# Performance work log

Measured on AMD Instinct MI355X. Metric: run time of the kernel, lower is better.

## Reference

```python
import jax, jax.numpy as jnp
import numpy as np


def setup_inputs() -> dict:
    key = jax.random.key(0)
    kx, kq, kk, kv = jax.random.split(key, 4)
    B, S, D = 4, 2048, 1024
    return {
        "x": jax.random.normal(kx, (B, S, D), dtype=jnp.float32),
        "Wq": jax.random.normal(kq, (D, D), dtype=jnp.float32),
        "Wk": jax.random.normal(kk, (D, D), dtype=jnp.float32),
        "Wv": jax.random.normal(kv, (D, D), dtype=jnp.float32),
    }


def reference(x, Wq, Wk, Wv):
    # x: [B, S, D]; single-head self-attention, output concat([x, attn], axis=-1)
    D = x.shape[-1]
    Q = jnp.einsum("bsd,de->bse", x, Wq)
    K = jnp.einsum("bsd,de->bse", x, Wk)
    V = jnp.einsum("bsd,de->bse", x, Wv)
    scale = 1.0 / jnp.sqrt(jnp.float32(D))
    scores = jax.nn.softmax(jnp.einsum("bqd,bkd->bqk", Q, K) * scale, axis=-1)  # [B,S,S]
    attn = jnp.einsum("bqk,bkd->bqd", scores, V)
    return jnp.concatenate([x, attn], axis=2)  # [B, S, 2D]
```

## Files before the change

### kernel.cpp

```cpp
#include <hip/hip_runtime.h>
#include <stdint.h>


typedef _Float16 h8 __attribute__((ext_vector_type(8)));
typedef _Float16 h4 __attribute__((ext_vector_type(4)));
typedef float    f4 __attribute__((ext_vector_type(4)));

#define BAR() __builtin_amdgcn_s_barrier()
#define LGKM0_FENCE()                                      \
  asm volatile("s_waitcnt lgkmcnt(0)" ::: "memory");       \
  __builtin_amdgcn_sched_barrier(0)

template <int N>
__device__ __forceinline__ void vmw() {
  if constexpr (N == 0)  asm volatile("s_waitcnt vmcnt(0)" ::: "memory");
  if constexpr (N == 1)  asm volatile("s_waitcnt vmcnt(1)" ::: "memory");
  if constexpr (N == 2)  asm volatile("s_waitcnt vmcnt(2)" ::: "memory");
  if constexpr (N == 3)  asm volatile("s_waitcnt vmcnt(3)" ::: "memory");
  if constexpr (N == 4)  asm volatile("s_waitcnt vmcnt(4)" ::: "memory");
  if constexpr (N == 5)  asm volatile("s_waitcnt vmcnt(5)" ::: "memory");
  if constexpr (N == 6)  asm volatile("s_waitcnt vmcnt(6)" ::: "memory");
  if constexpr (N == 7)  asm volatile("s_waitcnt vmcnt(7)" ::: "memory");
  if constexpr (N == 8)  asm volatile("s_waitcnt vmcnt(8)" ::: "memory");
  if constexpr (N == 9)  asm volatile("s_waitcnt vmcnt(9)" ::: "memory");
  if constexpr (N == 10) asm volatile("s_waitcnt vmcnt(10)" ::: "memory");
  if constexpr (N == 11) asm volatile("s_waitcnt vmcnt(11)" ::: "memory");
  if constexpr (N == 12) asm volatile("s_waitcnt vmcnt(12)" ::: "memory");
}

__device__ __forceinline__ void gl_lds16(const _Float16* g, _Float16* l) {
  __builtin_amdgcn_global_load_lds(
      (const __attribute__((address_space(1))) unsigned int*)g,
      (__attribute__((address_space(3))) unsigned int*)l, 16, 0, 0);
}

__global__ __launch_bounds__(256) void prep_x_split_copy(
    const float* __restrict__ x, _Float16* __restrict__ xh,
    _Float16* __restrict__ xl, float* __restrict__ out) {
  size_t i = (size_t)blockIdx.x * 256 + threadIdx.x;
  f4 v = ((const f4*)x)[i];
  h4 hi, lo;
#pragma unroll
  for (int j = 0; j < 4; ++j) {
    _Float16 h = (_Float16)v[j];
    hi[j] = h;
    lo[j] = (_Float16)(v[j] - (float)h);
  }
  ((h4*)xh)[i] = hi;
  ((h4*)xl)[i] = lo;
  size_t r = i >> 8, c = i & 255;
  ((f4*)out)[r * 512 + c] = v;
}

__global__ __launch_bounds__(256) void prep_w_noT(const float* __restrict__ W,
                                                  _Float16* __restrict__ Wh,
                                                  _Float16* __restrict__ Wl) {
  size_t i = (size_t)blockIdx.x * 256 + threadIdx.x;
  f4 v = ((const f4*)W)[i];
  h4 hi, lo;
#pragma unroll
  for (int j = 0; j < 4; ++j) {
    _Float16 h = (_Float16)v[j];
    hi[j] = h;
    lo[j] = (_Float16)(v[j] - (float)h);
  }
  ((h4*)Wh)[i] = hi;
  ((h4*)Wl)[i] = lo;
}

__global__ __launch_bounds__(256) void prep_w_T(const float* __restrict__ W,
                                                _Float16* __restrict__ WTh) {
  int i = blockIdx.x * 256 + threadIdx.x;
  int d = i >> 10, e = i & 1023;
  WTh[e * 1024 + d] = (_Float16)W[i];
}

enum { EM_F32 = 0, EM_QK = 1, EM_VT = 2 };

struct G8 {
  const _Float16* Areg[3]; long zA; int lda;
  const _Float16* Breg[4][3]; long zB; int ldb;
  int NT[4];
  int emode[4];
  float* Cf; long zC; int ldc; float scale;
  _Float16* Ch[4]; _Float16* Cl[4];
  _Float16* Vt;
};

template <int BM, int BN>
__global__ __launch_bounds__(512, 2) void gemmdp(G8 p) {
  constexpr int MFR = BM / 32;
  constexpr int MPH = MFR / 2;
  constexpr int NFR = BN / 64;
  constexpr int NPH = NFR / 2;
  constexpr int LA = BM / 128;
  constexpr int LB = BN / 128;
  __shared__ alignas(16) _Float16 ldsA[2][BM][64];
  __shared__ alignas(16) _Float16 ldsB[2][BN][64];

  const int t0 = threadIdx.x;
  const int lane = t0 & 63;
  const int w = t0 >> 6;
  const int wm = w >> 2, wn = w & 3;
  const int l15 = lane & 15, l4 = lane >> 4;

  const int nbx = gridDim.x, nby = gridDim.y;
  const int nwg = nbx * nby * gridDim.z;
  const int bid = blockIdx.x + nbx * (blockIdx.y + nby * blockIdx.z);
  const int nb = (bid & 7) * (nwg >> 3) + (bid >> 3);
  const int bx = nb % nbx, by = (nb / nbx) % nby, z = nb / (nbx * nby);

  const long Mb = (long)by * BM;
  const long Nb = (long)bx * BN;
  const int nt = p.NT[z];
  const long zAo = p.zA * z;
  const long zBo = p.zB * z;
  const int lda = p.lda, ldb = p.ldb;

  const int rr_lo = t0 >> 3;
  const int slot = t0 & 7;
  const int rr0_lo = (t0 & ~63) >> 3;

  f4 acc[MFR][NFR] = {};

  auto stageU = [&](int u, int sb, int kt) {
    const int k0 = kt << 6;
    const int r = k0 >> 10;
    const int cn = k0 & 1023;
    if (u == 0 || u == 3) {
      const _Float16* Ab = p.Areg[r] + zAo + cn;
      const int qm = (u == 3);
      constexpr int QS = BM / 4;
#pragma unroll
      for (int i = 0; i < LA; ++i) {
        int rr = i * 64 + rr_lo;
        int rr0 = i * 64 + rr0_lo;
        int row  = (rr  / QS) * (BM / 2) + qm * QS + (rr  % QS);
        int row0 = (rr0 / QS) * (BM / 2) + qm * QS + (rr0 % QS);
        int scol = (slot ^ (row & 7)) << 3;
        gl_lds16(Ab + (Mb + row) * (long)lda + scol, &ldsA[sb][row0][0]);
      }
    } else {
      const _Float16* Bb = p.Breg[z][r] + zBo + cn;
      const int hh = (u == 2);
      constexpr int BQ = BN / 8;
#pragma unroll
      for (int i = 0; i < LB; ++i) {
        int rr = i * 64 + rr_lo;
        int rr0 = i * 64 + rr0_lo;
        int row  = (rr  / BQ) * (BN / 4) + hh * BQ + (rr  % BQ);
        int row0 = (rr0 / BQ) * (BN / 4) + hh * BQ + (rr0 % BQ);
        int scol = (slot ^ (row & 7)) << 3;
        gl_lds16(Bb + (Nb + row) * (long)ldb + scol, &ldsB[sb][row0][0]);
      }
    }
  };

  h8 af[MPH][2];
  h8 bfh[2][NPH][2];

  auto dsA = [&](int qm, int buf) {
#pragma unroll
    for (int m = 0; m < MPH; ++m) {
      int row = wm * (BM / 2) + (qm * MPH + m) * 16 + l15;
#pragma unroll
      for (int ks = 0; ks < 2; ++ks)
        af[m][ks] = *(const h8*)&ldsA[buf][row][(((ks * 4 + l4) ^ (row & 7)) << 3)];
    }
  };
  auto dsB = [&](int hh, int buf) {
#pragma unroll
    for (int n = 0; n < NPH; ++n) {
      int row = wn * (16 * NFR) + (hh * NPH + n) * 16 + l15;
#pragma unroll
      for (int ks = 0; ks < 2; ++ks)
        bfh[hh][n][ks] = *(const h8*)&ldsB[buf][row][(((ks * 4 + l4) ^ (row & 7)) << 3)];
    }
  };
  auto mfmaQ = [&](int qm, int hh) {
    __builtin_amdgcn_s_setprio(1);
#pragma unroll
    for (int ks = 0; ks < 2; ++ks)
#pragma unroll
      for (int m = 0; m < MPH; ++m)
#pragma unroll
        for (int n = 0; n < NPH; ++n)
          acc[qm * MPH + m][hh * NPH + n] = __builtin_amdgcn_mfma_f32_16x16x32_f16(
              af[m][ks], bfh[hh][n][ks], acc[qm * MPH + m][hh * NPH + n], 0, 0, 0);
    __builtin_amdgcn_s_setprio(0);
  };

  constexpr int W_P0 = 3 * LA + 2 * LB;
  constexpr int W_P1 = 3 * LA + 3 * LB;
  constexpr int W_P3 = 3 * LA + 3 * LB;
  constexpr int TP0  = 3 * LA + 2 * LB;
  constexpr int TP1  = 2 * LA + 2 * LB;
  constexpr int TP3  = LA + LB;
  constexpr int UP0  = LA;

  stageU(0, 0, 0); stageU(1, 0, 0); stageU(2, 0, 0); stageU(3, 0, 0);
  stageU(0, 1, 1); stageU(1, 1, 1); stageU(2, 1, 1); stageU(3, 1, 1);
  vmw<W_P3>();
  BAR();

  int kt = 0;
  for (; kt + 2 < nt; ++kt) {
    const int buf = kt & 1;
    dsA(0, buf); dsB(0, buf);
    BAR(); LGKM0_FENCE();
    mfmaQ(0, 0);
    vmw<W_P0>(); BAR();
    dsB(1, buf);
    stageU(0, buf, kt + 2); stageU(1, buf, kt + 2);
    BAR(); LGKM0_FENCE();
    mfmaQ(0, 1);
    vmw<W_P1>(); BAR();
    dsA(1, buf);
    stageU(2, buf, kt + 2);
    BAR(); LGKM0_FENCE();
    mfmaQ(1, 1);
    BAR();
    stageU(3, buf, kt + 2);
    mfmaQ(1, 0);
    vmw<W_P3>(); BAR();
  }
  {
    const int buf = kt & 1;
    dsA(0, buf); dsB(0, buf);
    BAR(); LGKM0_FENCE();
    mfmaQ(0, 0);
    vmw<TP0>(); BAR();
    dsB(1, buf);
    BAR(); LGKM0_FENCE();
    mfmaQ(0, 1);
    vmw<TP1>(); BAR();
    dsA(1, buf);
    BAR(); LGKM0_FENCE();
    mfmaQ(1, 1);
    BAR();
    mfmaQ(1, 0);
    vmw<TP3>(); BAR();
    ++kt;
  }
  {
    const int buf = kt & 1;
    dsA(0, buf); dsB(0, buf);
    BAR(); LGKM0_FENCE();
    mfmaQ(0, 0);
    vmw<UP0>(); BAR();
    dsB(1, buf);
    BAR(); LGKM0_FENCE();
    mfmaQ(0, 1);
    vmw<0>(); BAR();
    dsA(1, buf);
    BAR(); LGKM0_FENCE();
    mfmaQ(1, 1);
    mfmaQ(1, 0);
  }

  const int em = p.emode[z];
  const long gr0 = wm * (BM / 2) + l4 * 4;
  const long gc0 = wn * (16 * NFR) + l15;
  if (em == EM_F32) {
    float* C = p.Cf + p.zC * z;
#pragma unroll
    for (int i = 0; i < MFR; ++i)
#pragma unroll
      for (int j = 0; j < NFR; ++j) {
        long gr = Mb + gr0 + i * 16;
        long gc = Nb + gc0 + j * 16;
#pragma unroll
        for (int r = 0; r < 4; ++r)
          C[(gr + r) * (long)p.ldc + gc] = acc[i][j][r] * p.scale;
      }
  } else if (em == EM_QK) {
    _Float16* Ch = p.Ch[z];
    _Float16* Cl = p.Cl[z];
#pragma unroll
    for (int i = 0; i < MFR; ++i)
#pragma unroll
      for (int j = 0; j < NFR; ++j) {
        long gr = Mb + gr0 + i * 16;
        long gc = Nb + gc0 + j * 16;
#pragma unroll
        for (int r = 0; r < 4; ++r) {
          float c = acc[i][j][r];
          _Float16 h = (_Float16)c;
          Ch[(gr + r) * 1024 + gc] = h;
          Cl[(gr + r) * 1024 + gc] = (_Float16)(c - (float)h);
        }
      }
  } else {
    _Float16* Vt = p.Vt;
#pragma unroll
    for (int i = 0; i < MFR; ++i)
#pragma unroll
      for (int j = 0; j < NFR; ++j) {
        long gr = Mb + gr0 + i * 16;
        long gc = Nb + gc0 + j * 16;
        long b = gr >> 11, s = gr & 2047;
        h4 hv;
#pragma unroll
        for (int r = 0; r < 4; ++r) hv[r] = (_Float16)acc[i][j][r];
        *(h4*)&Vt[b * (long)(1024 * 2048) + gc * 2048 + s] = hv;
      }
  }
}

__global__ __launch_bounds__(256) void softmax_rows(float* __restrict__ Sb) {
  const int t = threadIdx.x;
  float* row = Sb + (size_t)blockIdx.x * 2048;
  f4 v0 = ((const f4*)row)[t];
  f4 v1 = ((const f4*)row)[t + 256];
  float mx = -3.0e38f;
#pragma unroll
  for (int j = 0; j < 4; ++j) { mx = fmaxf(mx, v0[j]); mx = fmaxf(mx, v1[j]); }
#pragma unroll
  for (int o = 32; o > 0; o >>= 1) mx = fmaxf(mx, __shfl_xor(mx, o));
  __shared__ float red[4], red2[4];
  const int wave = t >> 6, lane = t & 63;
  if (lane == 0) red[wave] = mx;
  __syncthreads();
  mx = fmaxf(fmaxf(red[0], red[1]), fmaxf(red[2], red[3]));
  float pv[8];
  float sum = 0.f;
#pragma unroll
  for (int j = 0; j < 4; ++j) { pv[j] = __expf(v0[j] - mx); pv[4 + j] = __expf(v1[j] - mx); }
#pragma unroll
  for (int j = 0; j < 8; ++j) sum += pv[j];
#pragma unroll
  for (int o = 32; o > 0; o >>= 1) sum += __shfl_xor(sum, o);
  if (lane == 0) red2[wave] = sum;
  __syncthreads();
  sum = red2[0] + red2[1] + red2[2] + red2[3];
  float inv = 1.0f / sum;
  h4 o0, o1;
#pragma unroll
  for (int j = 0; j < 4; ++j) { o0[j] = (_Float16)(pv[j] * inv); o1[j] = (_Float16)(pv[4 + j] * inv); }
  _Float16* prow = (_Float16*)row;
  ((h4*)prow)[t] = o0;
  ((h4*)prow)[t + 256] = o1;
}

__global__ __launch_bounds__(256) void copy_x_half(const float* __restrict__ x,
                                                   float* __restrict__ out) {
  size_t i = (size_t)blockIdx.x * 256 + threadIdx.x;
  size_t r = i >> 8, c = i & 255;
  ((f4*)out)[r * 512 + c] = ((const f4*)x)[i];
}

__global__ void ws_sentinel(float* out, float v) { out[0] = v; }

extern "C" void kernel_launch(void* const* d_in, const int* in_sizes, int n_in,
                              void* d_out, int out_size, void* d_ws, size_t ws_size,
                              hipStream_t stream) {
  const float* x  = (const float*)d_in[0];
  const float* Wq = (const float*)d_in[1];
  const float* Wk = (const float*)d_in[2];
  const float* Wv = (const float*)d_in[3];
  float* out = (float*)d_out;

  const size_t MB = 1ull << 20;
  char* w = (char*)d_ws;
  _Float16* Th = (_Float16*)(w + 0 * MB);
  _Float16* Tl = (_Float16*)(w + 16 * MB);
  _Float16* xh = (_Float16*)(w + 32 * MB);
  _Float16* xl = (_Float16*)(w + 48 * MB);
  _Float16* VT = (_Float16*)(w + 64 * MB);
  float*    S  = (float*)   (w + 80 * MB);
  _Float16* Wqh = (_Float16*)(w + 80 * MB);
  _Float16* Wql = (_Float16*)(w + 82 * MB);
  _Float16* Wkh = (_Float16*)(w + 84 * MB);
  _Float16* Wkl = (_Float16*)(w + 86 * MB);
  _Float16* WvT = (_Float16*)(w + 88 * MB);
  _Float16* Nh  = (_Float16*)(w + 90 * MB);
  _Float16* Nl  = (_Float16*)(w + 92 * MB);

  if (ws_size < 144 * MB) {
    copy_x_half<<<8192, 256, 0, stream>>>(x, out);
    ws_sentinel<<<1, 1, 0, stream>>>(out, (float)ws_size);
    return;
  }

  prep_x_split_copy<<<8192, 256, 0, stream>>>(x, xh, xl, out);
  prep_w_noT<<<1024, 256, 0, stream>>>(Wq, Wqh, Wql);
  prep_w_noT<<<1024, 256, 0, stream>>>(Wk, Wkh, Wkl);
  prep_w_T<<<4096, 256, 0, stream>>>(Wv, WvT);

  G8 pn = {};
  pn.Areg[0] = Wkh; pn.Areg[1] = Wkl; pn.Areg[2] = Wkh; pn.zA = 0; pn.lda = 1024;
  pn.Breg[0][0] = Wqh; pn.Breg[0][1] = Wqh; pn.Breg[0][2] = Wql;
  pn.zB = 0; pn.ldb = 1024;
  pn.NT[0] = 48; pn.emode[0] = EM_QK;
  pn.Ch[0] = Nh; pn.Cl[0] = Nl;
  gemmdp<128, 128><<<dim3(8, 8, 1), 512, 0, stream>>>(pn);

  G8 pt = {};
  pt.Areg[0] = xh; pt.Areg[1] = xl; pt.Areg[2] = xh; pt.zA = 0; pt.lda = 1024;
  pt.Breg[0][0] = Nh; pt.Breg[0][1] = Nh; pt.Breg[0][2] = Nl;
  pt.zB = 0; pt.ldb = 1024;
  pt.NT[0] = 48; pt.emode[0] = EM_QK;
  pt.Ch[0] = Th; pt.Cl[0] = Tl;
  gemmdp<256, 128><<<dim3(8, 32, 1), 512, 0, stream>>>(pt);

  G8 pv = {};
  pv.Areg[0] = xh; pv.Areg[1] = xh; pv.Areg[2] = xh; pv.zA = 0; pv.lda = 1024;
  pv.Breg[0][0] = WvT; pv.Breg[0][1] = WvT; pv.Breg[0][2] = WvT;
  pv.zB = 0; pv.ldb = 1024;
  pv.NT[0] = 16; pv.emode[0] = EM_VT;
  pv.Vt = VT;
  gemmdp<128, 256><<<dim3(4, 64, 1), 512, 0, stream>>>(pv);

  G8 ps = {};
  ps.Areg[0] = Th; ps.Areg[1] = Tl; ps.Areg[2] = Th;
  ps.zA = 2048L * 1024; ps.lda = 1024;
  for (int zz = 0; zz < 4; ++zz) {
    ps.Breg[zz][0] = xh; ps.Breg[zz][1] = xh; ps.Breg[zz][2] = xl;
    ps.NT[zz] = 48; ps.emode[zz] = EM_F32;
  }
  ps.zB = 2048L * 1024; ps.ldb = 1024;
  ps.Cf = S; ps.zC = 2048L * 2048; ps.ldc = 2048; ps.scale = 0.03125f;
  gemmdp<256, 256><<<dim3(8, 8, 4), 512, 0, stream>>>(ps);

  softmax_rows<<<8192, 256, 0, stream>>>(S);

  G8 po = {};
  const _Float16* P = (const _Float16*)S;
  po.Areg[0] = P; po.Areg[1] = P + 1024; po.Areg[2] = P;
  po.zA = 2048L * 4096; po.lda = 4096;
  for (int zz = 0; zz < 4; ++zz) {
    po.Breg[zz][0] = VT; po.Breg[zz][1] = VT + 1024; po.Breg[zz][2] = VT;
    po.NT[zz] = 32; po.emode[zz] = EM_F32;
  }
  po.zB = 1024L * 2048; po.ldb = 2048;
  po.Cf = out + 1024; po.zC = 2048L * 2048; po.ldc = 2048; po.scale = 1.f;
  gemmdp<256, 128><<<dim3(8, 8, 4), 512, 0, stream>>>(po);
}
```

Before: 357.6 us.

## Split-K the Wk·Wq GEMM, restage pipeline prefetch, tile-transpose Wv, merge prep kernels

Several independent changes. The small Wk×Wq GEMM, previously 64 workgroups, is split along K into four partial fp32 products, which a new nsum kernel adds and splits into fp16 hi/lo parts. The main GEMM loop now prefetches stages one k-tile ahead with fewer outstanding loads and different waitcnt points. The Wv transpose uses an LDS-tiled kernel instead of scattered stores, the Wq/Wk prep kernels become one launch, and the T GEMM switches from 256x128 to 128x256 tiles. Split-K adds an extra launch and partial-sum traffic, and the shallower prefetch may expose more load latency.

```diff
diff --git a/kernel.cpp b/kernel.cpp
--- a/kernel.cpp
+++ b/kernel.cpp
@@ -13,19 +13,13 @@
 
 template <int N>
 __device__ __forceinline__ void vmw() {
-  if constexpr (N == 0)  asm volatile("s_waitcnt vmcnt(0)" ::: "memory");
-  if constexpr (N == 1)  asm volatile("s_waitcnt vmcnt(1)" ::: "memory");
-  if constexpr (N == 2)  asm volatile("s_waitcnt vmcnt(2)" ::: "memory");
-  if constexpr (N == 3)  asm volatile("s_waitcnt vmcnt(3)" ::: "memory");
-  if constexpr (N == 4)  asm volatile("s_waitcnt vmcnt(4)" ::: "memory");
-  if constexpr (N == 5)  asm volatile("s_waitcnt vmcnt(5)" ::: "memory");
-  if constexpr (N == 6)  asm volatile("s_waitcnt vmcnt(6)" ::: "memory");
-  if constexpr (N == 7)  asm volatile("s_waitcnt vmcnt(7)" ::: "memory");
-  if constexpr (N == 8)  asm volatile("s_waitcnt vmcnt(8)" ::: "memory");
-  if constexpr (N == 9)  asm volatile("s_waitcnt vmcnt(9)" ::: "memory");
-  if constexpr (N == 10) asm volatile("s_waitcnt vmcnt(10)" ::: "memory");
-  if constexpr (N == 11) asm volatile("s_waitcnt vmcnt(11)" ::: "memory");
-  if constexpr (N == 12) asm volatile("s_waitcnt vmcnt(12)" ::: "memory");
+  if constexpr (N == 0) asm volatile("s_waitcnt vmcnt(0)" ::: "memory");
+  if constexpr (N == 1) asm volatile("s_waitcnt vmcnt(1)" ::: "memory");
+  if constexpr (N == 2) asm volatile("s_waitcnt vmcnt(2)" ::: "memory");
+  if constexpr (N == 3) asm volatile("s_waitcnt vmcnt(3)" ::: "memory");
+  if constexpr (N == 4) asm volatile("s_waitcnt vmcnt(4)" ::: "memory");
+  if constexpr (N == 5) asm volatile("s_waitcnt vmcnt(5)" ::: "memory");
+  if constexpr (N == 6) asm volatile("s_waitcnt vmcnt(6)" ::: "memory");
 }
 
 __device__ __forceinline__ void gl_lds16(const _Float16* g, _Float16* l) {
@@ -52,9 +46,13 @@
   ((f4*)out)[r * 512 + c] = v;
 }
 
-__global__ __launch_bounds__(256) void prep_w_noT(const float* __restrict__ W,
-                                                  _Float16* __restrict__ Wh,
-                                                  _Float16* __restrict__ Wl) {
+__global__ __launch_bounds__(256) void prep_w2(
+    const float* __restrict__ Wq, const float* __restrict__ Wk,
+    _Float16* __restrict__ Wqh, _Float16* __restrict__ Wql,
+    _Float16* __restrict__ Wkh, _Float16* __restrict__ Wkl) {
+  const float* W = blockIdx.y ? Wk : Wq;
+  _Float16* Wh = blockIdx.y ? Wkh : Wqh;
+  _Float16* Wl = blockIdx.y ? Wkl : Wql;
   size_t i = (size_t)blockIdx.x * 256 + threadIdx.x;
   f4 v = ((const f4*)W)[i];
   h4 hi, lo;
@@ -68,11 +66,39 @@
   ((h4*)Wl)[i] = lo;
 }
 
-__global__ __launch_bounds__(256) void prep_w_T(const float* __restrict__ W,
-                                                _Float16* __restrict__ WTh) {
-  int i = blockIdx.x * 256 + threadIdx.x;
-  int d = i >> 10, e = i & 1023;
-  WTh[e * 1024 + d] = (_Float16)W[i];
+__global__ __launch_bounds__(256) void prep_wT(const float* __restrict__ W,
+                                               _Float16* __restrict__ WT) {
+  __shared__ float tl[32][33];
+  const int tc = blockIdx.x & 31;
+  const int tr = blockIdx.x >> 5;
+  const int r = threadIdx.x >> 3;
+  const int c4 = threadIdx.x & 7;
+  f4 v = *(const f4*)&W[(size_t)(tr * 32 + r) * 1024 + tc * 32 + c4 * 4];
+#pragma unroll
+  for (int j = 0; j < 4; ++j) tl[r][c4 * 4 + j] = v[j];
+  __syncthreads();
+  h4 o;
+#pragma unroll
+  for (int j = 0; j < 4; ++j) o[j] = (_Float16)tl[c4 * 4 + j][r];
+  *(h4*)&WT[(size_t)(tc * 32 + r) * 1024 + tr * 32 + c4 * 4] = o;
+}
+
+__global__ __launch_bounds__(256) void nsum(const float* __restrict__ Np,
+                                            _Float16* __restrict__ Nh,
+                                            _Float16* __restrict__ Nl) {
+  size_t i = (size_t)blockIdx.x * 256 + threadIdx.x;
+  const size_t M = 1024 * 1024 / 4;
+  f4 v = ((const f4*)Np)[i] + ((const f4*)Np)[i + M] +
+         ((const f4*)Np)[i + 2 * M] + ((const f4*)Np)[i + 3 * M];
+  h4 hi, lo;
+#pragma unroll
+  for (int j = 0; j < 4; ++j) {
+    _Float16 h = (_Float16)v[j];
+    hi[j] = h;
+    lo[j] = (_Float16)(v[j] - (float)h);
+  }
+  ((h4*)Nh)[i] = hi;
+  ((h4*)Nl)[i] = lo;
 }
 
 enum { EM_F32 = 0, EM_QK = 1, EM_VT = 2 };
@@ -81,6 +107,7 @@
   const _Float16* Areg[3]; long zA; int lda;
   const _Float16* Breg[4][3]; long zB; int ldb;
   int NT[4];
+  int KB[4];
   int emode[4];
   float* Cf; long zC; int ldc; float scale;
   _Float16* Ch[4]; _Float16* Cl[4];
@@ -113,6 +140,7 @@
   const long Mb = (long)by * BM;
   const long Nb = (long)bx * BN;
   const int nt = p.NT[z];
+  const int kb = p.KB[z];
   const long zAo = p.zA * z;
   const long zBo = p.zB * z;
   const int lda = p.lda, ldb = p.ldb;
@@ -124,7 +152,7 @@
   f4 acc[MFR][NFR] = {};
 
   auto stageU = [&](int u, int sb, int kt) {
-    const int k0 = kt << 6;
+    const int k0 = kb + (kt << 6);
     const int r = k0 >> 10;
     const int cn = k0 & 1023;
     if (u == 0 || u == 3) {
@@ -190,64 +218,62 @@
     __builtin_amdgcn_s_setprio(0);
   };
 
-  constexpr int W_P0 = 3 * LA + 2 * LB;
-  constexpr int W_P1 = 3 * LA + 3 * LB;
-  constexpr int W_P3 = 3 * LA + 3 * LB;
-  constexpr int TP0  = 3 * LA + 2 * LB;
-  constexpr int TP1  = 2 * LA + 2 * LB;
-  constexpr int TP3  = LA + LB;
-  constexpr int UP0  = LA;
+  constexpr int W1 = LA + 2 * LB;
+  constexpr int W3 = 2 * LA;
+  constexpr int WT3 = LA;
 
   stageU(0, 0, 0); stageU(1, 0, 0); stageU(2, 0, 0); stageU(3, 0, 0);
-  stageU(0, 1, 1); stageU(1, 1, 1); stageU(2, 1, 1); stageU(3, 1, 1);
-  vmw<W_P3>();
+  stageU(0, 1, 1);
+  vmw<W3>();
   BAR();
 
   int kt = 0;
   for (; kt + 2 < nt; ++kt) {
     const int buf = kt & 1;
+    stageU(1, buf ^ 1, kt + 1); stageU(2, buf ^ 1, kt + 1);
     dsA(0, buf); dsB(0, buf);
     BAR(); LGKM0_FENCE();
     mfmaQ(0, 0);
-    vmw<W_P0>(); BAR();
+    BAR();
     dsB(1, buf);
-    stageU(0, buf, kt + 2); stageU(1, buf, kt + 2);
     BAR(); LGKM0_FENCE();
     mfmaQ(0, 1);
-    vmw<W_P1>(); BAR();
+    vmw<W1>(); BAR();
+    stageU(3, buf ^ 1, kt + 1);
     dsA(1, buf);
-    stageU(2, buf, kt + 2);
     BAR(); LGKM0_FENCE();
     mfmaQ(1, 1);
     BAR();
-    stageU(3, buf, kt + 2);
+    stageU(0, buf, kt + 2);
     mfmaQ(1, 0);
-    vmw<W_P3>(); BAR();
+    vmw<W3>(); BAR();
+  }
+  {
+    const int buf = kt & 1;
+    stageU(1, buf ^ 1, kt + 1); stageU(2, buf ^ 1, kt + 1);
+    dsA(0, buf); dsB(0, buf);
+    BAR(); LGKM0_FENCE();
+    mfmaQ(0, 0);
+    BAR();
+    dsB(1, buf);
+    BAR(); LGKM0_FENCE();
+    mfmaQ(0, 1);
+    vmw<W1>(); BAR();
+    stageU(3, buf ^ 1, kt + 1);
+    dsA(1, buf);
+    BAR(); LGKM0_FENCE();
+    mfmaQ(1, 1);
+    BAR();
+    mfmaQ(1, 0);
+    vmw<WT3>(); BAR();
+    ++kt;
   }
   {
     const int buf = kt & 1;
     dsA(0, buf); dsB(0, buf);
     BAR(); LGKM0_FENCE();
     mfmaQ(0, 0);
-    vmw<TP0>(); BAR();
-    dsB(1, buf);
-    BAR(); LGKM0_FENCE();
-    mfmaQ(0, 1);
-    vmw<TP1>(); BAR();
-    dsA(1, buf);
-    BAR(); LGKM0_FENCE();
-    mfmaQ(1, 1);
     BAR();
-    mfmaQ(1, 0);
-    vmw<TP3>(); BAR();
-    ++kt;
-  }
-  {
-    const int buf = kt & 1;
-    dsA(0, buf); dsB(0, buf);
-    BAR(); LGKM0_FENCE();
-    mfmaQ(0, 0);
-    vmw<UP0>(); BAR();
     dsB(1, buf);
     BAR(); LGKM0_FENCE();
     mfmaQ(0, 1);
@@ -375,6 +401,7 @@
   _Float16* WvT = (_Float16*)(w + 88 * MB);
   _Float16* Nh  = (_Float16*)(w + 90 * MB);
   _Float16* Nl  = (_Float16*)(w + 92 * MB);
+  float*    Npart = (float*)(w + 96 * MB);
 
   if (ws_size < 144 * MB) {
     copy_x_half<<<8192, 256, 0, stream>>>(x, out);
@@ -383,17 +410,19 @@
   }
 
   prep_x_split_copy<<<8192, 256, 0, stream>>>(x, xh, xl, out);
-  prep_w_noT<<<1024, 256, 0, stream>>>(Wq, Wqh, Wql);
-  prep_w_noT<<<1024, 256, 0, stream>>>(Wk, Wkh, Wkl);
-  prep_w_T<<<4096, 256, 0, stream>>>(Wv, WvT);
+  prep_w2<<<dim3(1024, 2), 256, 0, stream>>>(Wq, Wk, Wqh, Wql, Wkh, Wkl);
+  prep_wT<<<1024, 256, 0, stream>>>(Wv, WvT);
 
   G8 pn = {};
   pn.Areg[0] = Wkh; pn.Areg[1] = Wkl; pn.Areg[2] = Wkh; pn.zA = 0; pn.lda = 1024;
-  pn.Breg[0][0] = Wqh; pn.Breg[0][1] = Wqh; pn.Breg[0][2] = Wql;
+  for (int zz = 0; zz < 4; ++zz) {
+    pn.Breg[zz][0] = Wqh; pn.Breg[zz][1] = Wqh; pn.Breg[zz][2] = Wql;
+    pn.NT[zz] = 12; pn.KB[zz] = zz * 768; pn.emode[zz] = EM_F32;
+  }
   pn.zB = 0; pn.ldb = 1024;
-  pn.NT[0] = 48; pn.emode[0] = EM_QK;
-  pn.Ch[0] = Nh; pn.Cl[0] = Nl;
-  gemmdp<128, 128><<<dim3(8, 8, 1), 512, 0, stream>>>(pn);
+  pn.Cf = Npart; pn.zC = 1024L * 1024; pn.ldc = 1024; pn.scale = 1.f;
+  gemmdp<128, 128><<<dim3(8, 8, 4), 512, 0, stream>>>(pn);
+  nsum<<<1024, 256, 0, stream>>>(Npart, Nh, Nl);
 
   G8 pt = {};
   pt.Areg[0] = xh; pt.Areg[1] = xl; pt.Areg[2] = xh; pt.zA = 0; pt.lda = 1024;
@@ -401,7 +430,7 @@
   pt.zB = 0; pt.ldb = 1024;
   pt.NT[0] = 48; pt.emode[0] = EM_QK;
   pt.Ch[0] = Th; pt.Cl[0] = Tl;
-  gemmdp<256, 128><<<dim3(8, 32, 1), 512, 0, stream>>>(pt);
+  gemmdp<128, 256><<<dim3(4, 64, 1), 512, 0, stream>>>(pt);
 
   G8 pv = {};
   pv.Areg[0] = xh; pv.Areg[1] = xh; pv.Areg[2] = xh; pv.zA = 0; pv.lda = 1024;
```

After: 370.8 us. 3.7% more time.
